# Performance work log

Hardware: AMD Instinct MI355X
Metric: run time of the kernel (lower is better)

Reference implementation:

```python
import jax, jax.numpy as jnp
import numpy as np

B, S, F, D = 64, 129, 768, 4
MOM = 0.9
EPS = 1e-6


def setup_inputs() -> dict:
    key = jax.random.key(0)
    ks = jax.random.split(key, 8)
    x = jax.random.normal(ks[0], (B, S, F), dtype=jnp.float32)
    labels = jax.random.randint(ks[1], (B,), 0, 16, dtype=jnp.int32)
    domain = jax.random.randint(ks[2], (B,), 0, D, dtype=jnp.int32)
    lmda = jax.random.beta(ks[3], 0.1, 0.1, (B, 1, 1)).astype(jnp.float32)
    d_rand = jax.random.randint(ks[4], (B,), 1, D, dtype=jnp.int32)  # range(1, num_domains)
    mean_buf = (0.1 * jax.random.normal(ks[5], (D, F))).astype(jnp.float32)
    var_buf = jax.random.uniform(ks[6], (D, F), minval=0.5, maxval=1.5, dtype=jnp.float32)
    hg_noise = jax.random.normal(ks[7], (B, S, F), dtype=jnp.float32)
    return {"input": x, "lmda": lmda, "mean_buf": mean_buf, "var_buf": var_buf,
            "hg_noise": hg_noise, "labels": labels, "domain": domain, "d_rand": d_rand}


def reference(input, lmda, mean_buf, var_buf, hg_noise, labels, domain, d_rand):
    x = input  # [B,S,F]
    b, s, f = x.shape
    d = mean_buf.shape[0]

    # --- per-domain mean/var over dims [0,1] (unbiased), momentum buffer update ---
    tok = x.reshape(b * s, f)
    seg = jnp.repeat(domain, s)  # [B*S]
    cnt = jax.ops.segment_sum(jnp.ones((b * s,), x.dtype), seg, num_segments=d)  # tokens/domain
    s1 = jax.ops.segment_sum(tok, seg, num_segments=d)          # [D,F]
    s2 = jax.ops.segment_sum(tok * tok, seg, num_segments=d)    # [D,F]
    n = cnt[:, None]
    mu_d = s1 / jnp.maximum(n, 1.0)
    var_d = (s2 - n * mu_d * mu_d) / jnp.maximum(n - 1.0, 1.0)  # unbiased, matches torch.var
    present = (cnt > 0)[:, None]
    new_mean = jnp.where(present, MOM * mean_buf + (1.0 - MOM) * mu_d, mean_buf)
    new_var = jnp.where(present, MOM * var_buf + (1.0 - MOM) * var_d, var_buf)

    # --- instance renorm over token dim (unbiased var) + cross-domain restyle ---
    mu_i = x.mean(1, keepdims=True)
    v_i = x.var(1, keepdims=True, ddof=1)
    x_normed = (x - mu_i) * jax.lax.rsqrt(v_i + EPS)
    ds = (domain + d_rand) % d
    x_new = x_normed * jnp.sqrt(new_var[ds] + EPS)[:, None, :] + new_mean[ds][:, None, :]
    x_mix = lmda * x + (1.0 - lmda) * x_new

    # --- Gaussian hallucinated samples from own-domain stats ---
    hg = new_mean[domain][:, None, :] + jnp.sqrt(new_var[domain] + EPS)[:, None, :] * hg_noise

    # --- pairwise euclidean distance + hard example mining + soft-margin triplet loss ---
    xe = jnp.concatenate([x, x_mix, hg], axis=0).reshape(3 * b, s * f)  # [3B, S*F]
    ln = jnp.concatenate([labels, labels, -jnp.ones((b,), labels.dtype)])
    sq = jnp.sum(xe * xe, axis=1)
    d2 = sq[:, None] + sq[None, :] - 2.0 * (xe @ xe.T)
    dist = jnp.sqrt(jnp.clip(d2, 1e-12))
    pos = ln[:, None] == ln[None, :]
    big = jnp.asarray(1e30, dist.dtype)
    dist_ap = jnp.max(jnp.where(pos, dist, -big), axis=1)
    dist_an = jnp.min(jnp.where(pos, big, dist), axis=1)
    tri_hard_loss = jnp.mean(jax.nn.softplus(dist_ap - dist_an))  # SoftMarginLoss, y=1

    return x_mix, tri_hard_loss, new_mean, new_var
```

## Files before the change

kernel.cpp:

```cpp
#include <hip/hip_runtime.h>
#include <math.h>

#define B_ 64
#define S_ 129
#define F_ 768
#define N3 192
#define GRID_MAIN 252
#define PSLICE_U 18432

#define WS_S1   0
#define WS_S2   49152
#define WS_SQ   98304
#define WS_PART 98560

#define OUT_LOSS 6340608
#define OUT_NM   6340609
#define OUT_NV   6343681

typedef unsigned int uint;
using short8v = __attribute__((ext_vector_type(8))) short;
using float4v = __attribute__((ext_vector_type(4))) float;

__device__ __forceinline__ uint pack2(float a, float b) {
    uint ua = __float_as_uint(a);
    uint ub = __float_as_uint(b);
    uint ha = (ua + 0x7FFFu + ((ua >> 16) & 1u)) >> 16;
    uint hb = (ub + 0x7FFFu + ((ub >> 16) & 1u)) & 0xFFFF0000u;
    return hb | ha;
}

__device__ __forceinline__ void bf16_store8(char* lds, int row, int g,
                                            float4 v0, float4 v1) {
    uint4 H;
    H.x = pack2(v0.x, v0.y);
    H.y = pack2(v0.z, v0.w);
    H.z = pack2(v1.x, v1.y);
    H.w = pack2(v1.z, v1.w);
    *(uint4*)(lds + row * 128 + ((g ^ (row & 7)) << 4)) = H;
}

__device__ __forceinline__ float4 fma4(float4 a, float4 x, float4 b) {
    float4 r;
    r.x = fmaf(a.x, x.x, b.x); r.y = fmaf(a.y, x.y, b.y);
    r.z = fmaf(a.z, x.z, b.z); r.w = fmaf(a.w, x.w, b.w);
    return r;
}

__global__ void k_stats(const float* __restrict__ x,
                        float* __restrict__ s1, float* __restrict__ s2,
                        float* __restrict__ sqw, float* __restrict__ out_loss) {
    __shared__ float4 r1[512], r2[512];
    if (blockIdx.x == 0) {
        if (threadIdx.x == 0) out_loss[0] = 0.0f;
        if (threadIdx.x < N3) sqw[threadIdx.x] = 0.0f;
    }
    int b = blockIdx.x / 3, fg = blockIdx.x % 3;
    int c = threadIdx.x & 63, sp = threadIdx.x >> 6;
    int f = fg * 256 + c * 4;
    const float* p = x + (size_t)b * S_ * F_ + f;
    int s0 = sp * 16;
    int se = s0 + 16 + (sp == 7 ? 1 : 0);
    float4 a1 = {0.f,0.f,0.f,0.f}, a2 = {0.f,0.f,0.f,0.f};
#pragma unroll 4
    for (int s = s0; s < se; ++s) {
        float4 v = *(const float4*)(p + s * F_);
        a1.x += v.x; a1.y += v.y; a1.z += v.z; a1.w += v.w;
        a2.x += v.x*v.x; a2.y += v.y*v.y; a2.z += v.z*v.z; a2.w += v.w*v.w;
    }
    r1[threadIdx.x] = a1; r2[threadIdx.x] = a2;
    __syncthreads();
    if (sp == 0) {
        float4 t1 = r1[c], t2 = r2[c];
#pragma unroll
        for (int k = 1; k < 8; ++k) {
            float4 u1 = r1[k * 64 + c], u2 = r2[k * 64 + c];
            t1.x += u1.x; t1.y += u1.y; t1.z += u1.z; t1.w += u1.w;
            t2.x += u2.x; t2.y += u2.y; t2.z += u2.z; t2.w += u2.w;
        }
        *(float4*)(s1 + b * F_ + f) = t1;
        *(float4*)(s2 + b * F_ + f) = t2;
    }
}

__global__ __launch_bounds__(512, 2)
void k_main(const float* __restrict__ x, const float* __restrict__ hgn,
            const float* __restrict__ s1, const float* __restrict__ s2,
            const float* __restrict__ mean_buf, const float* __restrict__ var_buf,
            const float* __restrict__ lmda, const int* __restrict__ domain,
            const int* __restrict__ d_rand,
            float* __restrict__ xmix, float* __restrict__ out_nm,
            float* __restrict__ out_nv,
            uint* __restrict__ part_u, float* __restrict__ sqw) {
    __shared__ __align__(16) char LDS[49152];
    __shared__ float NMV[4][64];
    __shared__ float SVV[4][64];

    int tid = threadIdx.x;
    int bid = blockIdx.x;
    int fc = bid % 12, sb = bid / 12;
    int f0 = fc * 64;
    int b = tid >> 3, g = tid & 7;
    int w = tid >> 6;
    int wr = (w >> 2) * 96, wc = (w & 3) * 48;
    int lane = tid & 63, m = lane & 15, qd = lane >> 4;

    size_t gA = ((size_t)b * S_ + sb) * F_ + f0 + (g << 3);
    float4 XA0 = ((const float4*)(x + gA))[0];
    float4 XA1 = ((const float4*)(x + gA))[1];
    float4 NA0 = ((const float4*)(hgn + gA))[0];
    float4 NA1 = ((const float4*)(hgn + gA))[1];
    size_t gB = ((size_t)b * S_ + sb + 21) * F_ + f0 + (g << 3);
    float4 XB0 = ((const float4*)(x + gB))[0];
    float4 XB1 = ((const float4*)(x + gB))[1];
    float4 NB0 = ((const float4*)(hgn + gB))[0];
    float4 NB1 = ((const float4*)(hgn + gB))[1];

    if (tid < 256) {
        int d = tid & 3, fl = tid >> 2;
        int f = f0 + fl;
        float a1 = 0.f, a2 = 0.f, cnt = 0.f;
#pragma unroll 8
        for (int bb = 0; bb < B_; ++bb) {
            bool mk = (domain[bb] == d);
            a1  += mk ? s1[bb * F_ + f] : 0.f;
            a2  += mk ? s2[bb * F_ + f] : 0.f;
            cnt += mk ? 1.f : 0.f;
        }
        float nm, nv;
        if (cnt > 0.f) {
            float n = cnt * (float)S_;
            float mu = a1 / n;
            float var = (a2 - n * mu * mu) / fmaxf(n - 1.f, 1.f);
            nm = 0.9f * mean_buf[d * F_ + f] + 0.1f * mu;
            nv = 0.9f * var_buf[d * F_ + f] + 0.1f * var;
        } else {
            nm = mean_buf[d * F_ + f];
            nv = var_buf[d * F_ + f];
        }
        NMV[d][fl] = nm;
        SVV[d][fl] = sqrtf(nv + 1e-6f);
        if (sb == 0) { out_nm[d * F_ + f] = nm; out_nv[d * F_ + f] = nv; }
    }
    __syncthreads();

    int cb = b * F_ + f0 + (g << 3);
    float4 S1a = ((const float4*)(s1 + cb))[0], S1b = ((const float4*)(s1 + cb))[1];
    float4 S2a = ((const float4*)(s2 + cb))[0], S2b = ((const float4*)(s2 + cb))[1];
    int dm = domain[b];
    int dsd = (dm + d_rand[b]) & 3;
    float lam = lmda[b];
    float4 C1a, C1b, C0a, C0b, HMa, HMb, HSa, HSb;
#define COEF(SC1, SC2, FL, RC1, RC0, RHM, RHS) {            \
        float mu = (SC1) * (1.0f / (float)S_);              \
        float v  = ((SC2) - (float)S_ * mu * mu) * (1.0f / (float)(S_ - 1)); \
        float r  = rsqrtf(v + 1e-6f);                       \
        float sv = SVV[dsd][FL];                            \
        float rs = r * sv;                                  \
        RC1 = lam + (1.0f - lam) * rs;                      \
        RC0 = (1.0f - lam) * (NMV[dsd][FL] - mu * rs);      \
        RHM = NMV[dm][FL];                                  \
        RHS = SVV[dm][FL]; }
    {
        int fb = g << 3;
        COEF(S1a.x, S2a.x, fb + 0, C1a.x, C0a.x, HMa.x, HSa.x);
        COEF(S1a.y, S2a.y, fb + 1, C1a.y, C0a.y, HMa.y, HSa.y);
        COEF(S1a.z, S2a.z, fb + 2, C1a.z, C0a.z, HMa.z, HSa.z);
        COEF(S1a.w, S2a.w, fb + 3, C1a.w, C0a.w, HMa.w, HSa.w);
        COEF(S1b.x, S2b.x, fb + 4, C1b.x, C0b.x, HMb.x, HSb.x);
        COEF(S1b.y, S2b.y, fb + 5, C1b.y, C0b.y, HMb.y, HSb.y);
        COEF(S1b.z, S2b.z, fb + 6, C1b.z, C0b.z, HMb.z, HSb.z);
        COEF(S1b.w, S2b.w, fb + 7, C1b.w, C0b.w, HMb.w, HSb.w);
    }
#undef COEF

    float4v acc[6][3];
#pragma unroll
    for (int i = 0; i < 6; ++i)
#pragma unroll
        for (int j = 0; j < 3; ++j)
            acc[i][j] = (float4v){0.f, 0.f, 0.f, 0.f};

#define STAGE_CHUNK(PL, X0_, X1_, N0_, N1_, GOFF_)                           \
    {                                                                        \
        float4 M0 = fma4(C1a, X0_, C0a);                                     \
        float4 M1 = fma4(C1b, X1_, C0b);                                     \
        ((float4*)(xmix + GOFF_))[0] = M0;                                   \
        ((float4*)(xmix + GOFF_))[1] = M1;                                   \
        float4 H0 = fma4(HSa, N0_, HMa);                                     \
        float4 H1 = fma4(HSb, N1_, HMb);                                     \
        bf16_store8(LDS, (PL) * 192 + b, g, X0_, X1_);                       \
        bf16_store8(LDS, (PL) * 192 + 64 + b, g, M0, M1);                    \
        bf16_store8(LDS, (PL) * 192 + 128 + b, g, H0, H1);                   \
    }

#define MFMA_PLANE(PL)                                                       \
        _Pragma("unroll")                                                    \
        for (int t = 0; t < 2; ++t) {                                        \
            short8v A[6];                                                    \
            _Pragma("unroll")                                                \
            for (int i = 0; i < 6; ++i) {                                    \
                int row = wr + i * 16 + m;                                   \
                int go = (((t << 2) + qd) ^ (row & 7)) << 4;                 \
                A[i] = *(const short8v*)(LDS + ((PL) * 192 + row) * 128 + go); \
            }                                                                \
            _Pragma("unroll")                                                \
            for (int j = 0; j < 3; ++j) {                                    \
                int row = wc + j * 16 + m;                                   \
                int go = (((t << 2) + qd) ^ (row & 7)) << 4;                 \
                short8v Bv = *(const short8v*)(LDS + ((PL) * 192 + row) * 128 + go); \
                _Pragma("unroll")                                            \
                for (int i = 0; i < 6; ++i)                                  \
                    acc[i][j] = __builtin_amdgcn_mfma_f32_16x16x32_bf16(     \
                        A[i], Bv, acc[i][j], 0, 0, 0);                       \
            }                                                                \
        }

    for (int s = sb; s < S_; s += 42) {
        bool haveB = (s + 21 < S_);
        STAGE_CHUNK(0, XA0, XA1, NA0, NA1, gA);
        if (haveB) STAGE_CHUNK(1, XB0, XB1, NB0, NB1, gB);
        __syncthreads();

        if (s + 42 < S_) {
            gA = ((size_t)b * S_ + s + 42) * F_ + f0 + (g << 3);
            XA0 = ((const float4*)(x + gA))[0];
            XA1 = ((const float4*)(x + gA))[1];
            NA0 = ((const float4*)(hgn + gA))[0];
            NA1 = ((const float4*)(hgn + gA))[1];
        }
        if (s + 63 < S_) {
            gB = ((size_t)b * S_ + s + 63) * F_ + f0 + (g << 3);
            XB0 = ((const float4*)(x + gB))[0];
            XB1 = ((const float4*)(x + gB))[1];
            NB0 = ((const float4*)(hgn + gB))[0];
            NB1 = ((const float4*)(hgn + gB))[1];
        }

        MFMA_PLANE(0);
        if (haveB) MFMA_PLANE(1);
        __syncthreads();
    }
#undef STAGE_CHUNK
#undef MFMA_PLANE

    float* T = (float*)LDS;
    const int PADW = 196;
    uint* dst = part_u + (size_t)bid * PSLICE_U;
    int lrb = (wr ? 16 : 0) + (qd << 2);
    int lr2 = tid >> 4;
#pragma unroll
    for (int i = 0; i < 6; ++i) {
        __syncthreads();
#pragma unroll
        for (int j = 0; j < 3; ++j) {
            int colb = wc + j * 16 + m;
#pragma unroll
            for (int r = 0; r < 4; ++r)
                T[(lrb + r) * PADW + colb] = acc[i][j][r];
        }
        __syncthreads();
        int grow = i * 16 + (lr2 & 15) + (lr2 >> 4) * 96;
#pragma unroll
        for (int k = 0; k < 3; ++k) {
            int c4 = k * 16 + (tid & 15);
            float4 vv = *(const float4*)&T[lr2 * PADW + (c4 << 2)];
            uint2 P;
            P.x = pack2(vv.x, vv.y);
            P.y = pack2(vv.z, vv.w);
            *(uint2*)(dst + grow * 96 + (c4 << 1)) = P;
        }
        if (tid < 32) {
            int dr = i * 16 + (tid & 15) + (tid >> 4) * 96;
            atomicAdd(sqw + dr, T[tid * PADW + dr]);
        }
    }
}

__global__ void k_loss(const uint* __restrict__ part_u, const float* __restrict__ sqw,
                       const int* __restrict__ labels,
                       float* __restrict__ out_loss) {
    __shared__ float ROW[2][N3];
    __shared__ float SQS[N3];
    __shared__ int   LN[N3];
    __shared__ float APW[3], ANW[3];
    int i = blockIdx.x, tid = threadIdx.x;
    if (tid < 384) {
        int c = tid % N3, h = tid / N3;
        int sh = (c & 1) << 4;
        const uint* prow = part_u + (size_t)i * 96 + (c >> 1);
        float sacc = 0.f;
#pragma unroll 4
        for (int p = h; p < GRID_MAIN; p += 2) {
            uint u = prow[(size_t)p * PSLICE_U];
            sacc += __uint_as_float(((u >> sh) & 0xFFFFu) << 16);
        }
        ROW[h][c] = sacc;
    }
    if (tid >= 320) {
        int c = tid - 320;
        SQS[c] = sqw[c];
        LN[c] = (c < 128) ? labels[c & 63] : -1;
    }
    __syncthreads();
    if (tid < N3) {
        float gij = ROW[0][tid] + ROW[1][tid];
        int li = LN[i];
        float d2 = SQS[i] + SQS[tid] - 2.0f * gij;
        float dist = sqrtf(fmaxf(d2, 1e-12f));
        bool pos = (li == LN[tid]);
        float ap = pos ? dist : -1e30f;
        float an = pos ? 1e30f : dist;
#pragma unroll
        for (int off = 32; off; off >>= 1) {
            ap = fmaxf(ap, __shfl_xor(ap, off));
            an = fminf(an, __shfl_xor(an, off));
        }
        if ((tid & 63) == 0) { APW[tid >> 6] = ap; ANW[tid >> 6] = an; }
    }
    __syncthreads();
    if (tid == 0) {
        float a = fmaxf(fmaxf(APW[0], APW[1]), APW[2]);
        float n = fminf(fminf(ANW[0], ANW[1]), ANW[2]);
        float xv = a - n;
        float sp = fmaxf(xv, 0.0f) + log1pf(expf(-fabsf(xv)));
        atomicAdd(out_loss, sp * (1.0f / (float)N3));
    }
}

extern "C" void kernel_launch(void* const* d_in, const int* in_sizes, int n_in,
                              void* d_out, int out_size, void* d_ws, size_t ws_size,
                              hipStream_t stream) {
    const float* x        = (const float*)d_in[0];
    const float* lmda     = (const float*)d_in[1];
    const float* mean_buf = (const float*)d_in[2];
    const float* var_buf  = (const float*)d_in[3];
    const float* hgn      = (const float*)d_in[4];
    const int*   labels   = (const int*)d_in[5];
    const int*   domain   = (const int*)d_in[6];
    const int*   d_rand   = (const int*)d_in[7];
    float* out = (float*)d_out;
    float* ws  = (float*)d_ws;

    float* sqw  = ws + WS_SQ;
    uint*  part = (uint*)(ws + WS_PART);

    k_stats<<<dim3(192), dim3(512), 0, stream>>>(x, ws + WS_S1, ws + WS_S2,
                                                 sqw, out + OUT_LOSS);
    k_main<<<dim3(GRID_MAIN), dim3(512), 0, stream>>>(
        x, hgn, ws + WS_S1, ws + WS_S2, mean_buf, var_buf,
        lmda, domain, d_rand,
        out, out + OUT_NM, out + OUT_NV, part, sqw);
    k_loss<<<dim3(N3), dim3(512), 0, stream>>>(part, sqw, labels,
                                               out + OUT_LOSS);
}
```

Before: 147.6 us.

## Double the main-kernel grid when workspace allows and store fp32 Gram partials

The token-row split in the main kernel becomes a runtime stride. When the workspace is large enough the grid doubles from 252 to 504 blocks, so more blocks are resident per CU and each block handles fewer rows. The per-block partial Gram tiles are now written as full fp32 instead of packed bf16, and the loss kernel sums a variable number of fp32 partials. This aims for better occupancy and more accurate partial sums. In exchange, partial-buffer write and read traffic grows two- to four-fold.

```diff
diff --git a/kernel.cpp b/kernel.cpp
--- a/kernel.cpp
+++ b/kernel.cpp
@@ -5,8 +5,7 @@
 #define S_ 129
 #define F_ 768
 #define N3 192
-#define GRID_MAIN 252
-#define PSLICE_U 18432
+#define GSZ 36864
 
 #define WS_S1   0
 #define WS_S2   49152
@@ -90,7 +89,7 @@
             const int* __restrict__ d_rand,
             float* __restrict__ xmix, float* __restrict__ out_nm,
             float* __restrict__ out_nv,
-            uint* __restrict__ part_u, float* __restrict__ sqw) {
+            float* __restrict__ part, float* __restrict__ sqw, int sg) {
     __shared__ __align__(16) char LDS[49152];
     __shared__ float NMV[4][64];
     __shared__ float SVV[4][64];
@@ -109,7 +108,7 @@
     float4 XA1 = ((const float4*)(x + gA))[1];
     float4 NA0 = ((const float4*)(hgn + gA))[0];
     float4 NA1 = ((const float4*)(hgn + gA))[1];
-    size_t gB = ((size_t)b * S_ + sb + 21) * F_ + f0 + (g << 3);
+    size_t gB = ((size_t)b * S_ + sb + sg) * F_ + f0 + (g << 3);
     float4 XB0 = ((const float4*)(x + gB))[0];
     float4 XB1 = ((const float4*)(x + gB))[1];
     float4 NB0 = ((const float4*)(hgn + gB))[0];
@@ -215,21 +214,21 @@
             }                                                                \
         }
 
-    for (int s = sb; s < S_; s += 42) {
-        bool haveB = (s + 21 < S_);
+    for (int s = sb; s < S_; s += 2 * sg) {
+        bool haveB = (s + sg < S_);
         STAGE_CHUNK(0, XA0, XA1, NA0, NA1, gA);
         if (haveB) STAGE_CHUNK(1, XB0, XB1, NB0, NB1, gB);
         __syncthreads();
 
-        if (s + 42 < S_) {
-            gA = ((size_t)b * S_ + s + 42) * F_ + f0 + (g << 3);
+        if (s + 2 * sg < S_) {
+            gA = ((size_t)b * S_ + s + 2 * sg) * F_ + f0 + (g << 3);
             XA0 = ((const float4*)(x + gA))[0];
             XA1 = ((const float4*)(x + gA))[1];
             NA0 = ((const float4*)(hgn + gA))[0];
             NA1 = ((const float4*)(hgn + gA))[1];
         }
-        if (s + 63 < S_) {
-            gB = ((size_t)b * S_ + s + 63) * F_ + f0 + (g << 3);
+        if (s + 3 * sg < S_) {
+            gB = ((size_t)b * S_ + s + 3 * sg) * F_ + f0 + (g << 3);
             XB0 = ((const float4*)(x + gB))[0];
             XB1 = ((const float4*)(x + gB))[1];
             NB0 = ((const float4*)(hgn + gB))[0];
@@ -245,7 +244,7 @@
 
     float* T = (float*)LDS;
     const int PADW = 196;
-    uint* dst = part_u + (size_t)bid * PSLICE_U;
+    float* dst = part + (size_t)bid * GSZ;
     int lrb = (wr ? 16 : 0) + (qd << 2);
     int lr2 = tid >> 4;
 #pragma unroll
@@ -264,10 +263,7 @@
         for (int k = 0; k < 3; ++k) {
             int c4 = k * 16 + (tid & 15);
             float4 vv = *(const float4*)&T[lr2 * PADW + (c4 << 2)];
-            uint2 P;
-            P.x = pack2(vv.x, vv.y);
-            P.y = pack2(vv.z, vv.w);
-            *(uint2*)(dst + grow * 96 + (c4 << 1)) = P;
+            *(float4*)(dst + grow * N3 + (c4 << 2)) = vv;
         }
         if (tid < 32) {
             int dr = i * 16 + (tid & 15) + (tid >> 4) * 96;
@@ -276,9 +272,9 @@
     }
 }
 
-__global__ void k_loss(const uint* __restrict__ part_u, const float* __restrict__ sqw,
+__global__ void k_loss(const float* __restrict__ part, const float* __restrict__ sqw,
                        const int* __restrict__ labels,
-                       float* __restrict__ out_loss) {
+                       float* __restrict__ out_loss, int npart) {
     __shared__ float ROW[2][N3];
     __shared__ float SQS[N3];
     __shared__ int   LN[N3];
@@ -286,14 +282,10 @@
     int i = blockIdx.x, tid = threadIdx.x;
     if (tid < 384) {
         int c = tid % N3, h = tid / N3;
-        int sh = (c & 1) << 4;
-        const uint* prow = part_u + (size_t)i * 96 + (c >> 1);
         float sacc = 0.f;
-#pragma unroll 4
-        for (int p = h; p < GRID_MAIN; p += 2) {
-            uint u = prow[(size_t)p * PSLICE_U];
-            sacc += __uint_as_float(((u >> sh) & 0xFFFFu) << 16);
-        }
+#pragma unroll 8
+        for (int p = h; p < npart; p += 2)
+            sacc += part[(size_t)p * GSZ + i * N3 + c];
         ROW[h][c] = sacc;
     }
     if (tid >= 320) {
@@ -342,14 +334,18 @@
     float* ws  = (float*)d_ws;
 
     float* sqw  = ws + WS_SQ;
-    uint*  part = (uint*)(ws + WS_PART);
+    float* part = ws + WS_PART;
+
+    long wsf = (long)(ws_size / 4);
+    int sg = (wsf >= WS_PART + 504L * GSZ) ? 42 : 21;
+    int grid = 12 * sg;
 
     k_stats<<<dim3(192), dim3(512), 0, stream>>>(x, ws + WS_S1, ws + WS_S2,
                                                  sqw, out + OUT_LOSS);
-    k_main<<<dim3(GRID_MAIN), dim3(512), 0, stream>>>(
+    k_main<<<dim3(grid), dim3(512), 0, stream>>>(
         x, hgn, ws + WS_S1, ws + WS_S2, mean_buf, var_buf,
         lmda, domain, d_rand,
-        out, out + OUT_NM, out + OUT_NV, part, sqw);
+        out, out + OUT_NM, out + OUT_NV, part, sqw, sg);
     k_loss<<<dim3(N3), dim3(512), 0, stream>>>(part, sqw, labels,
-                                               out + OUT_LOSS);
-}
+                                               out + OUT_LOSS, grid);
+}
```

Measured after the change: 161.9 us. +9.7%, slower.
